# Optimization experiments

Hardware: AMD Instinct MI355X
Metric: run time of the kernel (lower is better)

The kernel has to match this reference:

```python
import jax, jax.numpy as jnp
import numpy as np

N = 128          # number of nodes (particles)
NR = N * (N - 1) # number of directed edges, receiver-major order
B = 128          # batch
C = 16           # channel dim


def setup_inputs() -> dict:
    key = jax.random.key(0)
    x = jax.random.normal(key, (B, NR, C), dtype=jnp.float32)
    # assign_matrices enumerates (r, s) pairs receiver-major, so edge i has
    # receiver i // (N-1); Rr2 is the one-hot indicator of this mapping.
    receivers = jnp.arange(NR, dtype=jnp.int32) // (N - 1)
    return {"x": x, "receivers": receivers}


def reference(x, receivers):
    # exp of edge scores
    e = jnp.exp(x)  # [B, Nr, C]
    # tensordot(exp, Rr2, axes=[1,1]) == segment-sum over edges grouped by receiver
    seg = jax.ops.segment_sum(e.transpose(1, 0, 2), receivers, num_segments=N)  # [N, B, C]
    # tensordot(exp_sum, Rr2, axes=1) == gather each edge's receiver sum back to edges
    denom = seg[receivers]                 # [Nr, B, C]
    denom = denom.transpose(1, 2, 0)       # [B, C, Nr]
    # NOTE: the original divides the raw inputs (not exp) by the summed exp
    return x.transpose(0, 2, 1) / denom    # [B, C, Nr]
```

## Files before the change

### kernel.cpp

```cpp
#include <hip/hip_runtime.h>

#define NN   128
#define NE   127
#define CH   16
#define NRE  (NN * NE)

__global__ __launch_bounds__(256, 8) void attn2_kernel(const float* __restrict__ x,
                                                       float* __restrict__ out) {
    const int t   = threadIdx.x & 63;
    const int w   = threadIdx.x >> 6;
    const int seg = (blockIdx.x << 2) | w;
    const int b   = seg >> 7;
    const int r   = seg & (NN - 1);

    const float4* xs4 = (const float4*)(x + (size_t)seg * NE * CH);

    float4 v[8];
    #pragma unroll
    for (int it = 0; it < 8; ++it) {
        int f = t + (it << 6);
        v[it] = xs4[f < 508 ? f : 507];
    }

    float a0 = 0.f, a1 = 0.f, a2 = 0.f, a3 = 0.f;
    #pragma unroll
    for (int it = 0; it < 8; ++it) {
        int f = t + (it << 6);
        if (f < 508) {
            a0 += __expf(v[it].x); a1 += __expf(v[it].y);
            a2 += __expf(v[it].z); a3 += __expf(v[it].w);
        }
    }

    #pragma unroll
    for (int m = 4; m <= 32; m <<= 1) {
        a0 += __shfl_xor(a0, m, 64);
        a1 += __shfl_xor(a1, m, 64);
        a2 += __shfl_xor(a2, m, 64);
        a3 += __shfl_xor(a3, m, 64);
    }
    const float r0 = 1.0f / a0, r1 = 1.0f / a1, r2 = 1.0f / a2, r3 = 1.0f / a3;

    const int e1 = (t < 63) ? (t + 64) : 62;
    float4 p0[4], p1[4];
    #pragma unroll
    for (int j = 0; j < 4; ++j) p0[j] = xs4[(t  << 2) + j];
    #pragma unroll
    for (int j = 0; j < 4; ++j) p1[j] = xs4[(e1 << 2) + j];

    float4 rd[4];
    #pragma unroll
    for (int g = 0; g < 4; ++g) {
        const int src = (t & ~3) | g;
        rd[g].x = __shfl(r0, src, 64);
        rd[g].y = __shfl(r1, src, 64);
        rd[g].z = __shfl(r2, src, 64);
        rd[g].w = __shfl(r3, src, 64);
    }

    float* oseg = out + (size_t)b * CH * NRE + (size_t)r * NE;
    #pragma unroll
    for (int g = 0; g < 4; ++g) {
        #pragma unroll
        for (int i = 0; i < 4; ++i) {
            const int c = (g << 2) | i;
            const float rdc = ((const float*)&rd[g])[i];
            const float v0  = ((const float*)&p0[g])[i];
            const float v1  = ((const float*)&p1[g])[i];
            float* row = oseg + (size_t)c * NRE;
            row[t] = v0 * rdc;
            if (t < 63) row[64 + t] = v1 * rdc;
        }
    }
}

extern "C" void kernel_launch(void* const* d_in, const int* in_sizes, int n_in,
                              void* d_out, int out_size, void* d_ws, size_t ws_size,
                              hipStream_t stream) {
    const float* x = (const float*)d_in[0];
    float* out = (float*)d_out;
    attn2_kernel<<<(128 * 128) / 4, 256, 0, stream>>>(x, out);
}
```

Measured before the change: 253.2 us.

## Transpose through per-wave LDS tile and process two segments per wave

Each wave now writes its segment's values into a swizzled shared-memory tile while computing the exp sums, then reads the transposed values from LDS for the strided output stores. The second global re-read of x is removed. Each wave handles two segments, and the second segment's loads are issued before the first segment's stores to overlap memory traffic. The grid is halved and occupancy is lowered (launch bounds 8→5). LDS use goes up, and the inline s_waitcnt used as intra-wave ordering for tile reuse is fragile.

```diff
diff --git a/kernel.cpp b/kernel.cpp
--- a/kernel.cpp
+++ b/kernel.cpp
@@ -4,34 +4,27 @@
 #define NE   127
 #define CH   16
 #define NRE  (NN * NE)
+#define HALF 8192
+#define STR  128
 
-__global__ __launch_bounds__(256, 8) void attn2_kernel(const float* __restrict__ x,
-                                                       float* __restrict__ out) {
-    const int t   = threadIdx.x & 63;
-    const int w   = threadIdx.x >> 6;
-    const int seg = (blockIdx.x << 2) | w;
-    const int b   = seg >> 7;
-    const int r   = seg & (NN - 1);
-
-    const float4* xs4 = (const float4*)(x + (size_t)seg * NE * CH);
-
-    float4 v[8];
-    #pragma unroll
-    for (int it = 0; it < 8; ++it) {
-        int f = t + (it << 6);
-        v[it] = xs4[f < 508 ? f : 507];
-    }
-
+__device__ __forceinline__ void xpose_exp(float* __restrict__ T, const float4* v,
+                                          int t, int q, int er, int G,
+                                          float& r0, float& r1, float& r2, float& r3) {
+    const int p = q << 2;
     float a0 = 0.f, a1 = 0.f, a2 = 0.f, a3 = 0.f;
     #pragma unroll
     for (int it = 0; it < 8; ++it) {
         int f = t + (it << 6);
         if (f < 508) {
+            int es = (er + (it << 4)) ^ G;
+            T[(p + 0) * STR + es] = v[it].x;
+            T[(p + 1) * STR + es] = v[it].y;
+            T[(p + 2) * STR + es] = v[it].z;
+            T[(p + 3) * STR + es] = v[it].w;
             a0 += __expf(v[it].x); a1 += __expf(v[it].y);
             a2 += __expf(v[it].z); a3 += __expf(v[it].w);
         }
     }
-
     #pragma unroll
     for (int m = 4; m <= 32; m <<= 1) {
         a0 += __shfl_xor(a0, m, 64);
@@ -39,39 +32,76 @@
         a2 += __shfl_xor(a2, m, 64);
         a3 += __shfl_xor(a3, m, 64);
     }
-    const float r0 = 1.0f / a0, r1 = 1.0f / a1, r2 = 1.0f / a2, r3 = 1.0f / a3;
+    r0 = 1.0f / a0; r1 = 1.0f / a1; r2 = 1.0f / a2; r3 = 1.0f / a3;
+}
 
-    const int e1 = (t < 63) ? (t + 64) : 62;
-    float4 p0[4], p1[4];
-    #pragma unroll
-    for (int j = 0; j < 4; ++j) p0[j] = xs4[(t  << 2) + j];
-    #pragma unroll
-    for (int j = 0; j < 4; ++j) p1[j] = xs4[(e1 << 2) + j];
-
-    float4 rd[4];
+__device__ __forceinline__ void store_seg(const float* __restrict__ T, float* __restrict__ out,
+                                          int seg, int t,
+                                          float r0, float r1, float r2, float r3) {
+    const int b = seg >> 7;
+    const int r = seg & (NN - 1);
+    float* oseg = out + (size_t)b * CH * NRE + (size_t)r * NE;
     #pragma unroll
     for (int g = 0; g < 4; ++g) {
         const int src = (t & ~3) | g;
-        rd[g].x = __shfl(r0, src, 64);
-        rd[g].y = __shfl(r1, src, 64);
-        rd[g].z = __shfl(r2, src, 64);
-        rd[g].w = __shfl(r3, src, 64);
-    }
-
-    float* oseg = out + (size_t)b * CH * NRE + (size_t)r * NE;
-    #pragma unroll
-    for (int g = 0; g < 4; ++g) {
+        const float rc0 = __shfl(r0, src, 64);
+        const float rc1 = __shfl(r1, src, 64);
+        const float rc2 = __shfl(r2, src, 64);
+        const float rc3 = __shfl(r3, src, 64);
+        const float rc[4] = {rc0, rc1, rc2, rc3};
+        const int Gr = g << 4;
         #pragma unroll
         for (int i = 0; i < 4; ++i) {
             const int c = (g << 2) | i;
-            const float rdc = ((const float*)&rd[g])[i];
-            const float v0  = ((const float*)&p0[g])[i];
-            const float v1  = ((const float*)&p1[g])[i];
-            float* row = oseg + (size_t)c * NRE;
-            row[t] = v0 * rdc;
-            if (t < 63) row[64 + t] = v1 * rdc;
+            const float* row = T + c * STR;
+            float* orow = oseg + (size_t)c * NRE;
+            orow[t] = row[t ^ Gr] * rc[i];
+            if (t < 63) orow[64 + t] = row[(64 + t) ^ Gr] * rc[i];
         }
     }
+}
+
+__global__ __launch_bounds__(256, 5) void attn2_kernel(const float* __restrict__ x,
+                                                       float* __restrict__ out) {
+    __shared__ float tile[4][CH * STR];
+
+    const int t  = threadIdx.x & 63;
+    const int w  = threadIdx.x >> 6;
+    const int q  = t & 3;
+    const int er = t >> 2;
+    const int G  = q << 4;
+
+    float* T = tile[w];
+
+    const int segA = (blockIdx.x << 2) | w;
+    const int segB = segA + HALF;
+
+    const float4* xA = (const float4*)(x + (size_t)segA * NE * CH);
+    const float4* xB = (const float4*)(x + (size_t)segB * NE * CH);
+
+    float4 v[8];
+    #pragma unroll
+    for (int it = 0; it < 8; ++it) {
+        int f = t + (it << 6);
+        v[it] = xA[f < 508 ? f : 507];
+    }
+    float a0, a1, a2, a3;
+    xpose_exp(T, v, t, q, er, G, a0, a1, a2, a3);
+
+    float4 v2[8];
+    #pragma unroll
+    for (int it = 0; it < 8; ++it) {
+        int f = t + (it << 6);
+        v2[it] = xB[f < 508 ? f : 507];
+    }
+
+    store_seg(T, out, segA, t, a0, a1, a2, a3);
+
+    asm volatile("s_waitcnt lgkmcnt(0)" ::: "memory");
+
+    float b0, b1, b2, b3;
+    xpose_exp(T, v2, t, q, er, G, b0, b1, b2, b3);
+    store_seg(T, out, segB, t, b0, b1, b2, b3);
 }
 
 extern "C" void kernel_launch(void* const* d_in, const int* in_sizes, int n_in,
@@ -79,5 +109,5 @@
                               hipStream_t stream) {
     const float* x = (const float*)d_in[0];
     float* out = (float*)d_out;
-    attn2_kernel<<<(128 * 128) / 4, 256, 0, stream>>>(x, out);
+    attn2_kernel<<<HALF / 4, 256, 0, stream>>>(x, out);
 }
```

Result: faster. 239.2 us (-5.6%).
